# Kernel optimization log

Measured on AMD Instinct MI355X. Metric: run time of the kernel, lower is better.

## Reference

```python
import jax, jax.numpy as jnp
import numpy as np

N_NODES = 100000
N_EDGES = 1600000


def sage_conv(x, src, dst, Wl, Wr, b, num_nodes):
    # mean-aggregate neighbor (source) features at targets, then linear + root
    msg = x[src]  # [E, F] gather
    agg = jax.ops.segment_sum(msg, dst, num_segments=num_nodes)
    deg = jax.ops.segment_sum(jnp.ones((src.shape[0],), dtype=x.dtype), dst, num_segments=num_nodes)
    mean = agg / jnp.maximum(deg, 1.0)[:, None]
    return mean @ Wl.T + x @ Wr.T + b


def setup_inputs() -> dict:
    key = jax.random.key(0)
    ks = jax.random.split(key, 12)
    nf, h, h2, nc = 128, 64, 128, 64

    def w(k, o, i):
        return jax.random.normal(k, (o, i), dtype=jnp.float32) * (1.0 / np.sqrt(i))

    return {
        "x": jax.random.normal(ks[0], (N_NODES, nf), dtype=jnp.float32),
        "edge_index": jax.random.randint(ks[1], (2, N_EDGES), 0, N_NODES, dtype=jnp.int64),
        "Wl1": w(ks[2], h, nf), "Wr1": w(ks[3], h, nf),
        "b1": jnp.zeros((h,), dtype=jnp.float32),
        "Wl2": w(ks[4], h2, h), "Wr2": w(ks[5], h2, h),
        "b2": jnp.zeros((h2,), dtype=jnp.float32),
        "Wl3": w(ks[6], nc, h2), "Wr3": w(ks[7], nc, h2),
        "b3": jnp.zeros((nc,), dtype=jnp.float32),
    }


def reference(x, edge_index, Wl1, Wr1, b1, Wl2, Wr2, b2, Wl3, Wr3, b3):
    src, dst = edge_index[0], edge_index[1]
    n = x.shape[0]
    h = sage_conv(x, src, dst, Wl1, Wr1, b1, n)
    h = jax.nn.relu(h)  # dropout is identity in eval mode
    h = sage_conv(h, src, dst, Wl2, Wr2, b2, n)
    h = jax.nn.relu(h)
    out = sage_conv(h, src, dst, Wl3, Wr3, b3, n)
    return out
```

## Files before the change

kernel.cpp:

```cpp
#include <hip/hip_runtime.h>

#define THREADS 256
#define BSHIFT 7
#define BNODES 128
#define CHUNK 8192
#define BTHREADS 1024
#define CAP 4096

typedef __attribute__((ext_vector_type(8))) short short8;
typedef __attribute__((ext_vector_type(4))) float f32x4;
typedef __attribute__((ext_vector_type(4))) unsigned int u32x4;

__device__ inline unsigned short f2bf(float f) {
  unsigned int u = __float_as_uint(f);
  unsigned int r = u + 0x7fffu + ((u >> 16) & 1u);
  return (unsigned short)(r >> 16);
}


__global__ __launch_bounds__(1024) void init_bcur(int* __restrict__ bcur, int NBK) {
  int t = threadIdx.x;
  if (t < NBK) bcur[t] = t * CAP;
}

__global__ __launch_bounds__(BTHREADS) void fill_block(
    const int* __restrict__ src, const int* __restrict__ dst,
    int* __restrict__ bcur, unsigned* __restrict__ bins, int E, int NBK) {
  __shared__ int lcnt[1024];
  __shared__ int lbase[1024];
  int t = threadIdx.x;
  lcnt[t] = 0;
  __syncthreads();
  int base = blockIdx.x * CHUNK;
  unsigned recs[CHUNK / BTHREADS];
  int bkt[CHUNK / BTHREADS];
#pragma unroll
  for (int i = 0; i < CHUNK / BTHREADS; ++i) {
    int e = base + i * BTHREADS + t;
    if (e < E) {
      int d = dst[e];
      bkt[i] = d >> BSHIFT;
      recs[i] = ((unsigned)(d & (BNODES - 1)) << 17) | (unsigned)src[e];
      atomicAdd(&lcnt[bkt[i]], 1);
    } else bkt[i] = -1;
  }
  __syncthreads();
  if (t < NBK) {
    int c = lcnt[t];
    lbase[t] = (c > 0) ? atomicAdd(&bcur[t], c) : 0;
  }
  __syncthreads();
  lcnt[t] = 0;
  __syncthreads();
#pragma unroll
  for (int i = 0; i < CHUNK / BTHREADS; ++i) {
    if (bkt[i] >= 0) {
      int pos = lbase[bkt[i]] + atomicAdd(&lcnt[bkt[i]], 1);
      if (pos < (bkt[i] + 1) * CAP) bins[pos] = recs[i];
    }
  }
}

__global__ __launch_bounds__(256) void bucket_csr(
    const unsigned* __restrict__ bins, const int* __restrict__ bcur,
    int* __restrict__ rowbeg, int* __restrict__ rowend, float* __restrict__ invdeg,
    int* __restrict__ adj, int N) {
  __shared__ int lcnt[BNODES];
  __shared__ int lscan[BNODES];
  __shared__ int lrow[BNODES];
  __shared__ int lcur[BNODES];
  int b = blockIdx.x, t = threadIdx.x;
  if (t < BNODES) { lcnt[t] = 0; lcur[t] = 0; }
  __syncthreads();
  int beg = b * CAP;
  int end = bcur[b];
  if (end > (b + 1) * CAP) end = (b + 1) * CAP;
  for (int i = beg + t; i < end; i += 256) atomicAdd(&lcnt[bins[i] >> 17], 1);
  __syncthreads();
  if (t < BNODES) lscan[t] = lcnt[t];
  __syncthreads();
  for (int d = 1; d < BNODES; d <<= 1) {
    int v = (t < BNODES && t >= d) ? lscan[t - d] : 0;
    __syncthreads();
    if (t < BNODES) lscan[t] += v;
    __syncthreads();
  }
  if (t < BNODES) {
    int ro = b * CAP + lscan[t] - lcnt[t];
    lrow[t] = ro;
    int g = b * BNODES + t;
    if (g < N) {
      rowbeg[g] = ro;
      rowend[g] = ro + lcnt[t];
      invdeg[g] = 1.0f / (float)(lcnt[t] > 1 ? lcnt[t] : 1);
    }
  }
  __syncthreads();
  for (int i = beg + t; i < end; i += 256) {
    unsigned v = bins[i];
    int n = v >> 17;
    int pos = atomicAdd(&lcur[n], 1);
    adj[lrow[n] + pos] = (int)(v & 0x1FFFFu);
  }
}


__global__ __launch_bounds__(256) void mfma_gemm(
    const void* __restrict__ A0_, const void* __restrict__ A1_, int sa0b, int sa1b, int a_fp32,
    const float* __restrict__ W0, const float* __restrict__ W1, int wmode,
    const float* __restrict__ bias, int relu,
    unsigned short* __restrict__ out0, unsigned short* __restrict__ out1,
    int so0, int so1, int N)
{
  __shared__ __align__(16) unsigned char Wlds[128 * 256];
  int t = threadIdx.x;

#pragma unroll
  for (int it = 0; it < 8; ++it) {
    int i = it * 256 + t;
    int c = i >> 4, kg = i & 15;
    const float* src;
    if (wmode == 0) src = (c < 64) ? (W0 + c * 128 + kg * 8) : (W1 + (c - 64) * 128 + kg * 8);
    else            src = (kg < 8) ? (W0 + c * 64 + kg * 8)  : (W1 + c * 64 + (kg - 8) * 8);
    short8 v;
#pragma unroll
    for (int q = 0; q < 8; ++q) v[q] = (short)f2bf(src[q]);
    *(short8*)(&Wlds[c * 256 + ((kg * 16) ^ ((c & 7) << 4))]) = v;
  }
  __syncthreads();

  int w = t >> 6, l = t & 63;
  int lr = l & 15, lk = l >> 4;
  int r0 = blockIdx.x * 128 + w * 32;

  short8 afr[2][4];
#pragma unroll
  for (int set = 0; set < 2; ++set) {
    int row = r0 + set * 16 + lr;
    bool ok = row < N;
    if (a_fp32) {
#pragma unroll
      for (int kt = 0; kt < 4; ++kt) {
        short8 a = {0, 0, 0, 0, 0, 0, 0, 0};
        if (ok) {
          const unsigned char* bp = (const unsigned char*)(kt < 2 ? A0_ : A1_)
                + (size_t)row * (kt < 2 ? sa0b : sa1b) + 32 * lk + 128 * (kt & 1);
          f32x4 f0 = *(const f32x4*)bp;
          f32x4 f1 = *(const f32x4*)(bp + 16);
#pragma unroll
          for (int q = 0; q < 4; ++q) { a[q] = (short)f2bf(f0[q]); a[q + 4] = (short)f2bf(f1[q]); }
        }
        afr[set][kt] = a;
      }
    } else {
#pragma unroll
      for (int kt = 0; kt < 4; ++kt) {
        short8 a = {0, 0, 0, 0, 0, 0, 0, 0};
        if (ok) {
          const unsigned char* bp = (const unsigned char*)(kt < 2 ? A0_ : A1_)
                + (size_t)row * (kt < 2 ? sa0b : sa1b) + 16 * lk + 64 * (kt & 1);
          a = *(const short8*)bp;
        }
        afr[set][kt] = a;
      }
    }
  }

  f32x4 acc[2][8];
#pragma unroll
  for (int s = 0; s < 2; ++s)
#pragma unroll
    for (int c = 0; c < 8; ++c) acc[s][c] = (f32x4){0.f, 0.f, 0.f, 0.f};

#pragma unroll
  for (int ct = 0; ct < 8; ++ct) {
    int c = ct * 16 + lr;
    const unsigned char* rowp = &Wlds[c * 256];
    unsigned swz = (unsigned)((c & 7) << 4);
    short8 bfr[4];
#pragma unroll
    for (int kt = 0; kt < 4; ++kt)
      bfr[kt] = *(const short8*)(rowp + (((unsigned)(16 * lk + 64 * kt)) ^ swz));
#pragma unroll
    for (int kt = 0; kt < 4; ++kt) {
      acc[0][ct] = __builtin_amdgcn_mfma_f32_16x16x32_bf16(afr[0][kt], bfr[kt], acc[0][ct], 0, 0, 0);
      acc[1][ct] = __builtin_amdgcn_mfma_f32_16x16x32_bf16(afr[1][kt], bfr[kt], acc[1][ct], 0, 0, 0);
    }
  }

#pragma unroll
  for (int set = 0; set < 2; ++set) {
    int rbase = r0 + set * 16 + lk * 4;
#pragma unroll
    for (int ct = 0; ct < 8; ++ct) {
      int col = ct * 16 + lr;
      unsigned short* outp = (col < 64) ? out0 : out1;
      int so = (col < 64) ? so0 : so1;
      int cb = (col < 64) ? col : col - 64;
      float bv = bias ? bias[col] : 0.f;
#pragma unroll
      for (int j = 0; j < 4; ++j) {
        int row = rbase + j;
        if (row < N) {
          float v = acc[set][ct][j] + bv;
          if (relu) v = fmaxf(v, 0.f);
          outp[(size_t)row * so + cb] = f2bf(v);
        }
      }
    }
  }
}


__global__ __launch_bounds__(256) void agg_bf16(
    const unsigned short* __restrict__ feat, const int* __restrict__ adj,
    const int* __restrict__ rowbeg, const int* __restrict__ rowend,
    const float* __restrict__ invdeg,
    const unsigned short* __restrict__ add, const float* __restrict__ bias,
    void* __restrict__ outv, int N, int relu, int out_fp32)
{
  int t = threadIdx.x;
  int lane = t & 63;
  int g8 = lane >> 3, sl = lane & 7;
  int node = blockIdx.x * 32 + (t >> 6) * 8 + g8;
  if (node >= N) return;
  int beg = rowbeg[node], end = rowend[node];
  float s0 = 0.f, s1 = 0.f, s2 = 0.f, s3 = 0.f;
  float s4 = 0.f, s5 = 0.f, s6 = 0.f, s7 = 0.f;
  int j = beg;
  for (; j + 8 <= end; j += 8) {
    u32x4 p[8];
#pragma unroll
    for (int u = 0; u < 8; ++u)
      p[u] = *(const u32x4*)(feat + (size_t)adj[j + u] * 64 + 8 * sl);
#pragma unroll
    for (int u = 0; u < 8; ++u) {
      s0 += __uint_as_float(p[u].x << 16); s1 += __uint_as_float(p[u].x & 0xffff0000u);
      s2 += __uint_as_float(p[u].y << 16); s3 += __uint_as_float(p[u].y & 0xffff0000u);
      s4 += __uint_as_float(p[u].z << 16); s5 += __uint_as_float(p[u].z & 0xffff0000u);
      s6 += __uint_as_float(p[u].w << 16); s7 += __uint_as_float(p[u].w & 0xffff0000u);
    }
  }
  for (; j < end; ++j) {
    u32x4 p = *(const u32x4*)(feat + (size_t)adj[j] * 64 + 8 * sl);
    s0 += __uint_as_float(p.x << 16); s1 += __uint_as_float(p.x & 0xffff0000u);
    s2 += __uint_as_float(p.y << 16); s3 += __uint_as_float(p.y & 0xffff0000u);
    s4 += __uint_as_float(p.z << 16); s5 += __uint_as_float(p.z & 0xffff0000u);
    s6 += __uint_as_float(p.w << 16); s7 += __uint_as_float(p.w & 0xffff0000u);
  }
  float inv = invdeg[node];
  s0 *= inv; s1 *= inv; s2 *= inv; s3 *= inv;
  s4 *= inv; s5 *= inv; s6 *= inv; s7 *= inv;
  if (add) {
    u32x4 q = *(const u32x4*)(add + (size_t)node * 64 + 8 * sl);
    s0 += __uint_as_float(q.x << 16); s1 += __uint_as_float(q.x & 0xffff0000u);
    s2 += __uint_as_float(q.y << 16); s3 += __uint_as_float(q.y & 0xffff0000u);
    s4 += __uint_as_float(q.z << 16); s5 += __uint_as_float(q.z & 0xffff0000u);
    s6 += __uint_as_float(q.w << 16); s7 += __uint_as_float(q.w & 0xffff0000u);
  }
  if (bias) {
    f32x4 b0 = *(const f32x4*)(bias + 8 * sl);
    f32x4 b1 = *(const f32x4*)(bias + 8 * sl + 4);
    s0 += b0[0]; s1 += b0[1]; s2 += b0[2]; s3 += b0[3];
    s4 += b1[0]; s5 += b1[1]; s6 += b1[2]; s7 += b1[3];
  }
  if (relu) {
    s0 = fmaxf(s0, 0.f); s1 = fmaxf(s1, 0.f); s2 = fmaxf(s2, 0.f); s3 = fmaxf(s3, 0.f);
    s4 = fmaxf(s4, 0.f); s5 = fmaxf(s5, 0.f); s6 = fmaxf(s6, 0.f); s7 = fmaxf(s7, 0.f);
  }
  if (out_fp32) {
    float* o = (float*)outv + (size_t)node * 64 + 8 * sl;
    *(f32x4*)o       = (f32x4){s0, s1, s2, s3};
    *(f32x4*)(o + 4) = (f32x4){s4, s5, s6, s7};
  } else {
    u32x4 pk;
    pk.x = ((unsigned)f2bf(s1) << 16) | (unsigned)f2bf(s0);
    pk.y = ((unsigned)f2bf(s3) << 16) | (unsigned)f2bf(s2);
    pk.z = ((unsigned)f2bf(s5) << 16) | (unsigned)f2bf(s4);
    pk.w = ((unsigned)f2bf(s7) << 16) | (unsigned)f2bf(s6);
    *(u32x4*)((unsigned short*)outv + (size_t)node * 64 + 8 * sl) = pk;
  }
}


extern "C" void kernel_launch(void* const* d_in, const int* in_sizes, int n_in,
                              void* d_out, int out_size, void* d_ws, size_t ws_size,
                              hipStream_t stream) {
  const float* x   = (const float*)d_in[0];
  const int* edges = (const int*)d_in[1];
  const float* Wl1 = (const float*)d_in[2];
  const float* Wr1 = (const float*)d_in[3];
  const float* b1  = (const float*)d_in[4];
  const float* Wl2 = (const float*)d_in[5];
  const float* Wr2 = (const float*)d_in[6];
  const float* b2  = (const float*)d_in[7];
  const float* Wl3 = (const float*)d_in[8];
  const float* Wr3 = (const float*)d_in[9];
  const float* b3  = (const float*)d_in[10];

  int N = in_sizes[0] / 128;
  int E = in_sizes[1] / 2;
  const int* srcp = edges;
  const int* dstp = edges + E;
  int NBK = (N + BNODES - 1) / BNODES;

  char* ws = (char*)d_ws;
  size_t off = 0;
  auto carve = [&](size_t bytes) -> void* {
    void* p = (void*)(ws + off);
    off += (bytes + 255) & ~(size_t)255;
    return p;
  };
  unsigned* bins = (unsigned*)carve((size_t)NBK * CAP * 4);
  int*   adj    = (int*)carve((size_t)NBK * CAP * 4);
  int*   rowbeg = (int*)carve((size_t)N * 4);
  int*   rowend = (int*)carve((size_t)N * 4);
  int*   bcur   = (int*)carve(1024 * 4);
  float* invdeg = (float*)carve((size_t)N * 4);
  unsigned short* B1 = (unsigned short*)carve((size_t)N * 64 * 2);
  unsigned short* B2 = (unsigned short*)carve((size_t)N * 64 * 2);
  unsigned short* B3 = (unsigned short*)carve((size_t)N * 64 * 2);
  unsigned short* P  = (unsigned short*)carve((size_t)N * 128 * 2);
  (void)ws_size;

  int gridF = (E + CHUNK - 1) / CHUNK;

  init_bcur<<<1, 1024, 0, stream>>>(bcur, NBK);
  fill_block<<<gridF, BTHREADS, 0, stream>>>(srcp, dstp, bcur, bins, E, NBK);
  bucket_csr<<<NBK, THREADS, 0, stream>>>(bins, bcur, rowbeg, rowend, invdeg, adj, N);

  int gridG = (N + 127) / 128;
  int gridA = (N + 31) / 32;

  mfma_gemm<<<gridG, THREADS, 0, stream>>>(x, x + 64, 512, 512, 1, Wl1, Wr1, 0,
                                           nullptr, 0, B1, B2, 64, 64, N);
  agg_bf16<<<gridA, THREADS, 0, stream>>>(B1, adj, rowbeg, rowend, invdeg, B2, b1, B3, N, 1, 0);
  agg_bf16<<<gridA, THREADS, 0, stream>>>(B3, adj, rowbeg, rowend, invdeg, nullptr, nullptr, B1, N, 0, 0);
  mfma_gemm<<<gridG, THREADS, 0, stream>>>(B1, B3, 128, 128, 0, Wl2, Wr2, 1,
                                           b2, 1, P, P + 64, 128, 128, N);
  mfma_gemm<<<gridG, THREADS, 0, stream>>>(P, P + 64, 256, 256, 0, Wl3, Wr3, 0,
                                           nullptr, 0, B2, B1, 64, 64, N);
  agg_bf16<<<gridA, THREADS, 0, stream>>>(B2, adj, rowbeg, rowend, invdeg, B1, b3, d_out, N, 0, 1);
}
```

Before: 216.7 us.

## Fuse edge binning with first GEMM and sort adjacency by source range

Merges the edge-bucketing fill kernel and the first layer GEMM into one launch, with block index selecting the role, so the two independent jobs overlap and a launch is removed. The fill uses smaller 256-thread chunks. bucket_csr now counting-sorts each bucket on 1024 sub-keys combining target node and high source bits, so each node's neighbor list is grouped by source range to improve gather locality in aggregation. The cost is more shared memory and a larger scan in bucket_csr.

```diff
diff --git a/kernel.cpp b/kernel.cpp
--- a/kernel.cpp
+++ b/kernel.cpp
@@ -3,8 +3,7 @@
 #define THREADS 256
 #define BSHIFT 7
 #define BNODES 128
-#define CHUNK 8192
-#define BTHREADS 1024
+#define CHUNK2 2048
 #define CAP 4096
 
 typedef __attribute__((ext_vector_type(8))) short short8;
@@ -23,20 +22,21 @@
   if (t < NBK) bcur[t] = t * CAP;
 }
 
-__global__ __launch_bounds__(BTHREADS) void fill_block(
-    const int* __restrict__ src, const int* __restrict__ dst,
-    int* __restrict__ bcur, unsigned* __restrict__ bins, int E, int NBK) {
-  __shared__ int lcnt[1024];
-  __shared__ int lbase[1024];
+__device__ void fill_dev(unsigned char* smem, int bid,
+                         const int* __restrict__ src, const int* __restrict__ dst,
+                         int* __restrict__ bcur, unsigned* __restrict__ bins,
+                         int E, int NBK) {
+  int* lcnt  = (int*)smem;
+  int* lbase = (int*)(smem + 4096);
   int t = threadIdx.x;
-  lcnt[t] = 0;
-  __syncthreads();
-  int base = blockIdx.x * CHUNK;
-  unsigned recs[CHUNK / BTHREADS];
-  int bkt[CHUNK / BTHREADS];
-#pragma unroll
-  for (int i = 0; i < CHUNK / BTHREADS; ++i) {
-    int e = base + i * BTHREADS + t;
+  for (int i = t; i < NBK; i += 256) lcnt[i] = 0;
+  __syncthreads();
+  int base = bid * CHUNK2;
+  unsigned recs[8];
+  int bkt[8];
+#pragma unroll
+  for (int i = 0; i < 8; ++i) {
+    int e = base + i * 256 + t;
     if (e < E) {
       int d = dst[e];
       bkt[i] = d >> BSHIFT;
@@ -45,15 +45,15 @@
     } else bkt[i] = -1;
   }
   __syncthreads();
-  if (t < NBK) {
-    int c = lcnt[t];
-    lbase[t] = (c > 0) ? atomicAdd(&bcur[t], c) : 0;
-  }
-  __syncthreads();
-  lcnt[t] = 0;
-  __syncthreads();
-#pragma unroll
-  for (int i = 0; i < CHUNK / BTHREADS; ++i) {
+  for (int i = t; i < NBK; i += 256) {
+    int c = lcnt[i];
+    lbase[i] = (c > 0) ? atomicAdd(&bcur[i], c) : 0;
+  }
+  __syncthreads();
+  for (int i = t; i < NBK; i += 256) lcnt[i] = 0;
+  __syncthreads();
+#pragma unroll
+  for (int i = 0; i < 8; ++i) {
     if (bkt[i] >= 0) {
       int pos = lbase[bkt[i]] + atomicAdd(&lcnt[bkt[i]], 1);
       if (pos < (bkt[i] + 1) * CAP) bins[pos] = recs[i];
@@ -65,56 +65,64 @@
     const unsigned* __restrict__ bins, const int* __restrict__ bcur,
     int* __restrict__ rowbeg, int* __restrict__ rowend, float* __restrict__ invdeg,
     int* __restrict__ adj, int N) {
-  __shared__ int lcnt[BNODES];
-  __shared__ int lscan[BNODES];
-  __shared__ int lrow[BNODES];
-  __shared__ int lcur[BNODES];
+  __shared__ int lcnt[1024];
+  __shared__ int lrow[1024];
+  __shared__ int lcur[1024];
+  __shared__ int lpart[256];
   int b = blockIdx.x, t = threadIdx.x;
-  if (t < BNODES) { lcnt[t] = 0; lcur[t] = 0; }
+  for (int i = t; i < 1024; i += 256) { lcnt[i] = 0; lcur[i] = 0; }
   __syncthreads();
   int beg = b * CAP;
   int end = bcur[b];
-  if (end > (b + 1) * CAP) end = (b + 1) * CAP;
-  for (int i = beg + t; i < end; i += 256) atomicAdd(&lcnt[bins[i] >> 17], 1);
-  __syncthreads();
-  if (t < BNODES) lscan[t] = lcnt[t];
-  __syncthreads();
-  for (int d = 1; d < BNODES; d <<= 1) {
-    int v = (t < BNODES && t >= d) ? lscan[t - d] : 0;
+  if (end > beg + CAP) end = beg + CAP;
+  for (int i = beg + t; i < end; i += 256)
+    atomicAdd(&lcnt[(bins[i] >> 14) & 1023], 1);
+  __syncthreads();
+  int c0 = lcnt[4 * t], c1 = lcnt[4 * t + 1], c2 = lcnt[4 * t + 2], c3 = lcnt[4 * t + 3];
+  int tot = c0 + c1 + c2 + c3;
+  lpart[t] = tot;
+  __syncthreads();
+  for (int d = 1; d < 256; d <<= 1) {
+    int x = (t >= d) ? lpart[t - d] : 0;
     __syncthreads();
-    if (t < BNODES) lscan[t] += v;
+    lpart[t] += x;
     __syncthreads();
   }
+  int pre = lpart[t] - tot;
+  lrow[4 * t]     = beg + pre;
+  lrow[4 * t + 1] = beg + pre + c0;
+  lrow[4 * t + 2] = beg + pre + c0 + c1;
+  lrow[4 * t + 3] = beg + pre + c0 + c1 + c2;
+  __syncthreads();
   if (t < BNODES) {
-    int ro = b * CAP + lscan[t] - lcnt[t];
-    lrow[t] = ro;
     int g = b * BNODES + t;
     if (g < N) {
-      rowbeg[g] = ro;
-      rowend[g] = ro + lcnt[t];
-      invdeg[g] = 1.0f / (float)(lcnt[t] > 1 ? lcnt[t] : 1);
+      int rb = lrow[t * 8];
+      int re = lrow[t * 8 + 7] + lcnt[t * 8 + 7];
+      rowbeg[g] = rb;
+      rowend[g] = re;
+      int dgr = re - rb;
+      invdeg[g] = 1.0f / (float)(dgr > 1 ? dgr : 1);
     }
   }
   __syncthreads();
   for (int i = beg + t; i < end; i += 256) {
     unsigned v = bins[i];
-    int n = v >> 17;
-    int pos = atomicAdd(&lcur[n], 1);
-    adj[lrow[n] + pos] = (int)(v & 0x1FFFFu);
-  }
-}
-
-
-__global__ __launch_bounds__(256) void mfma_gemm(
+    int key = (v >> 14) & 1023;
+    int pos = atomicAdd(&lcur[key], 1);
+    adj[lrow[key] + pos] = (int)(v & 0x1FFFFu);
+  }
+}
+
+
+__device__ void gemm_dev(unsigned char* Wlds, int bid,
     const void* __restrict__ A0_, const void* __restrict__ A1_, int sa0b, int sa1b, int a_fp32,
     const float* __restrict__ W0, const float* __restrict__ W1, int wmode,
     const float* __restrict__ bias, int relu,
     unsigned short* __restrict__ out0, unsigned short* __restrict__ out1,
     int so0, int so1, int N)
 {
-  __shared__ __align__(16) unsigned char Wlds[128 * 256];
   int t = threadIdx.x;
-
 #pragma unroll
   for (int it = 0; it < 8; ++it) {
     int i = it * 256 + t;
@@ -131,7 +139,7 @@
 
   int w = t >> 6, l = t & 63;
   int lr = l & 15, lk = l >> 4;
-  int r0 = blockIdx.x * 128 + w * 32;
+  int r0 = bid * 128 + w * 32;
 
   short8 afr[2][4];
 #pragma unroll
@@ -209,6 +217,30 @@
       }
     }
   }
+}
+
+__global__ __launch_bounds__(256) void mfma_gemm(
+    const void* A0_, const void* A1_, int sa0b, int sa1b, int a_fp32,
+    const float* W0, const float* W1, int wmode, const float* bias, int relu,
+    unsigned short* out0, unsigned short* out1, int so0, int so1, int N)
+{
+  __shared__ __align__(16) unsigned char smem[128 * 256];
+  gemm_dev(smem, blockIdx.x, A0_, A1_, sa0b, sa1b, a_fp32, W0, W1, wmode,
+           bias, relu, out0, out1, so0, so1, N);
+}
+
+__global__ __launch_bounds__(256) void k1_fill_gemm(
+    const int* src, const int* dst, int* bcur, unsigned* bins, int E, int NBK, int gridF,
+    const void* A0_, const void* A1_, int sa0b, int sa1b,
+    const float* W0, const float* W1,
+    unsigned short* out0, unsigned short* out1, int so0, int so1, int N)
+{
+  __shared__ __align__(16) unsigned char smem[128 * 256];
+  if (blockIdx.x < gridF)
+    fill_dev(smem, blockIdx.x, src, dst, bcur, bins, E, NBK);
+  else
+    gemm_dev(smem, blockIdx.x - gridF, A0_, A1_, sa0b, sa1b, 1, W0, W1, 0,
+             nullptr, 0, out0, out1, so0, so1, N);
 }
 
 
@@ -323,17 +355,18 @@
   unsigned short* P  = (unsigned short*)carve((size_t)N * 128 * 2);
   (void)ws_size;
 
-  int gridF = (E + CHUNK - 1) / CHUNK;
-
-  init_bcur<<<1, 1024, 0, stream>>>(bcur, NBK);
-  fill_block<<<gridF, BTHREADS, 0, stream>>>(srcp, dstp, bcur, bins, E, NBK);
-  bucket_csr<<<NBK, THREADS, 0, stream>>>(bins, bcur, rowbeg, rowend, invdeg, adj, N);
-
+  int gridF = (E + CHUNK2 - 1) / CHUNK2;
   int gridG = (N + 127) / 128;
   int gridA = (N + 31) / 32;
 
-  mfma_gemm<<<gridG, THREADS, 0, stream>>>(x, x + 64, 512, 512, 1, Wl1, Wr1, 0,
-                                           nullptr, 0, B1, B2, 64, 64, N);
+  init_bcur<<<1, 1024, 0, stream>>>(bcur, NBK);
+
+  k1_fill_gemm<<<gridF + gridG, THREADS, 0, stream>>>(
+      srcp, dstp, bcur, bins, E, NBK, gridF,
+      x, x + 64, 512, 512, Wl1, Wr1, B1, B2, 64, 64, N);
+
+  bucket_csr<<<NBK, THREADS, 0, stream>>>(bins, bcur, rowbeg, rowend, invdeg, adj, N);
+
   agg_bf16<<<gridA, THREADS, 0, stream>>>(B1, adj, rowbeg, rowend, invdeg, B2, b1, B3, N, 1, 0);
   agg_bf16<<<gridA, THREADS, 0, stream>>>(B3, adj, rowbeg, rowend, invdeg, nullptr, nullptr, B1, N, 0, 0);
   mfma_gemm<<<gridG, THREADS, 0, stream>>>(B1, B3, 128, 128, 0, Wl2, Wr2, 1,
```

After: 261.8 us. 1.21x slower.
